# Kernel tuning notes

Measured on AMD Instinct MI355X. Metric: run time of the kernel, lower is better.

The kernel has to match this reference:

```python
import jax, jax.numpy as jnp
import numpy as np

PI = jnp.float32(3.14159265359)  # same truncated constant as the torch source
LOG_2PI = jnp.log(2.0 * PI)
STAB = 0.001  # covariance stabilizer added before inversion in the original


def _decoder(z, W1, b1, W2, b2, W3, b3, W4, b4):
    # f: Linear(z_dim,64)-ELU-Linear(64,128)-ELU-Linear(128,256)-ELU-Linear(256,784)-Sigmoid
    h = jax.nn.elu(z @ W1.T + b1)
    h = jax.nn.elu(h @ W2.T + b2)
    h = jax.nn.elu(h @ W3.T + b3)
    return jax.nn.sigmoid(h @ W4.T + b4)


def setup_inputs() -> dict:
    key = jax.random.key(0)
    ks = jax.random.split(key, 6)
    N, K, D, Z = 512, 256, 784, 2

    def lin(k, fan_in, fan_out):
        k1, k2 = jax.random.split(k)
        lim = 1.0 / np.sqrt(fan_in)
        W = jax.random.uniform(k1, (fan_out, fan_in), minval=-lim, maxval=lim, dtype=jnp.float32)
        b = jax.random.uniform(k2, (fan_out,), minval=-lim, maxval=lim, dtype=jnp.float32)
        return W, b

    W1, b1 = lin(ks[0], Z, 64)
    W2, b2 = lin(ks[1], 64, 128)
    W3, b3 = lin(ks[2], 128, 256)
    W4, b4 = lin(ks[3], 256, D)
    X = jax.random.uniform(ks[4], (N, D), dtype=jnp.float32)   # image pixels in [0,1)
    z = jax.random.normal(ks[5], (K, Z), dtype=jnp.float32)    # latent MC samples
    log_std = jnp.zeros((1,), dtype=jnp.float32)               # self.log_std_ = tensor([0.0])
    return dict(X=X, z=z, log_std=log_std, W1=W1, b1=b1, W2=W2, b2=b2,
                W3=W3, b3=b3, W4=W4, b4=b4)


def reference(X, z, log_std, W1, b1, W2, b2, W3, b3, W4, b4):
    # expected_log_likelihood(X, z) == objective(X, z, variational=False)
    N, D = X.shape
    K, Z = z.shape
    s = jnp.exp(log_std[0])  # isotropic likelihood variance (covariance = s * I_D)

    # --- log_likelihood: MVN log-prob with covariance s*I_D (closed form of det/inverse) ---
    params = _decoder(z, W1, b1, W2, b2, W3, b3, W4, b4)           # (K, D)
    diffs = X[:, None, :] - params[None, :, :]                      # (N, K, D) dominant traffic
    quad = jnp.sum(diffs * diffs, axis=-1) / (s + STAB)             # inv((s+eps)*I) = I/(s+eps)
    log_norm = -0.5 * D * LOG_2PI - 0.5 * (D * log_std[0])          # log det(s*I_D) = D*log s
    ll = log_norm - 0.5 * quad                                      # (N, K)

    # --- log_prior: MVN log-prob with identity covariance (stabilized inverse: I/1.001) ---
    log_prior = -0.5 * Z * LOG_2PI - 0.5 * jnp.sum(z * z, axis=-1) / (1.0 + STAB)  # (K,)

    # --- importance weights computed under no_grad in the original ---
    sg = jax.lax.stop_gradient
    ll_c = sg(ll)
    lp_c = sg(log_prior)
    m = jnp.max(ll_c)
    ll_s = ll_c - m                                                 # (N, K)
    log_joint_s = ll_s + lp_c[None, :]                              # (N, K)
    evidence_s = jnp.exp(ll_s).sum(axis=-1) / K                     # (N,)
    log_evidence_s = jnp.log(evidence_s)
    log_posteriors = (log_joint_s - log_evidence_s[:, None]).T      # (K, N)
    iw = jnp.exp(log_posteriors - lp_c[:, None])                    # (K, N), constants

    ell = (iw.T * ll).sum(axis=-1) / K                              # (N,)
    return ell.sum() / N
```

## Files before the change

kernel.cpp:

```cpp
#include <hip/hip_runtime.h>
#include <math.h>

#define LOG_2PI 1.8378770664093453f

__device__ __forceinline__ float elu_f(float x) {
    return x > 0.0f ? x : expm1f(x);
}
__device__ __forceinline__ float sigmoid_f(float x) {
    return 1.0f / (1.0f + expf(-x));
}

__global__ __launch_bounds__(256) void decoder_kernel(
    const float* __restrict__ z,
    const float* __restrict__ W1, const float* __restrict__ b1,
    const float* __restrict__ W2, const float* __restrict__ b2,
    const float* __restrict__ W3, const float* __restrict__ b3,
    const float* __restrict__ W4, const float* __restrict__ b4,
    float* __restrict__ PT)
{
    __shared__ __align__(16) float h1[4][64];
    __shared__ __align__(16) float h2[4][128];
    __shared__ __align__(16) float h3[4][256];

    const int t  = threadIdx.x;
    const int kt = blockIdx.x >> 2;
    const int jq = blockIdx.x & 3;
    const int k0 = kt * 4;

    {
        int kl = t >> 6, o = t & 63;
        float z0 = z[(k0 + kl) * 2 + 0];
        float z1 = z[(k0 + kl) * 2 + 1];
        float v = fmaf(z0, W1[o * 2 + 0], fmaf(z1, W1[o * 2 + 1], b1[o]));
        h1[kl][o] = elu_f(v);
    }
    __syncthreads();

    for (int idx = t; idx < 512; idx += 256) {
        int kl = idx >> 7, o = idx & 127;
        const float4* wr = reinterpret_cast<const float4*>(W2 + o * 64);
        const float4* hr = reinterpret_cast<const float4*>(h1[kl]);
        float acc = b2[o];
        #pragma unroll
        for (int i = 0; i < 16; ++i) {
            float4 w = wr[i]; float4 a = hr[i];
            acc = fmaf(w.x, a.x, acc); acc = fmaf(w.y, a.y, acc);
            acc = fmaf(w.z, a.z, acc); acc = fmaf(w.w, a.w, acc);
        }
        h2[kl][o] = elu_f(acc);
    }
    __syncthreads();

    for (int idx = t; idx < 1024; idx += 256) {
        int kl = idx >> 8, o = idx & 255;
        const float4* wr = reinterpret_cast<const float4*>(W3 + o * 128);
        const float4* hr = reinterpret_cast<const float4*>(h2[kl]);
        float acc = b3[o];
        #pragma unroll
        for (int i = 0; i < 32; ++i) {
            float4 w = wr[i]; float4 a = hr[i];
            acc = fmaf(w.x, a.x, acc); acc = fmaf(w.y, a.y, acc);
            acc = fmaf(w.z, a.z, acc); acc = fmaf(w.w, a.w, acc);
        }
        h3[kl][o] = elu_f(acc);
    }
    __syncthreads();

    if (t < 196) {
        const int j = jq * 196 + t;
        const float4* wr = reinterpret_cast<const float4*>(W4 + j * 256);
        const float4* h0 = reinterpret_cast<const float4*>(h3[0]);
        const float4* hA = reinterpret_cast<const float4*>(h3[1]);
        const float4* hB = reinterpret_cast<const float4*>(h3[2]);
        const float4* hC = reinterpret_cast<const float4*>(h3[3]);
        float bb = b4[j];
        float a0 = bb, a1 = bb, a2 = bb, a3 = bb;
        #pragma unroll 8
        for (int i = 0; i < 64; ++i) {
            float4 w = wr[i];
            float4 x0 = h0[i], x1 = hA[i], x2 = hB[i], x3 = hC[i];
            a0 = fmaf(w.x, x0.x, a0); a0 = fmaf(w.y, x0.y, a0);
            a0 = fmaf(w.z, x0.z, a0); a0 = fmaf(w.w, x0.w, a0);
            a1 = fmaf(w.x, x1.x, a1); a1 = fmaf(w.y, x1.y, a1);
            a1 = fmaf(w.z, x1.z, a1); a1 = fmaf(w.w, x1.w, a1);
            a2 = fmaf(w.x, x2.x, a2); a2 = fmaf(w.y, x2.y, a2);
            a2 = fmaf(w.z, x2.z, a2); a2 = fmaf(w.w, x2.w, a2);
            a3 = fmaf(w.x, x3.x, a3); a3 = fmaf(w.y, x3.y, a3);
            a3 = fmaf(w.z, x3.z, a3); a3 = fmaf(w.w, x3.w, a3);
        }
        float4 r = make_float4(sigmoid_f(a0), sigmoid_f(a1),
                               sigmoid_f(a2), sigmoid_f(a3));
        *reinterpret_cast<float4*>(PT + j * 256 + k0) = r;
    }
}

__global__ __launch_bounds__(256) void quad_part_kernel(
    const float* __restrict__ X, const float* __restrict__ log_std,
    const float* __restrict__ PT, float* __restrict__ part)
{
    __shared__ __align__(16) float Xs[4][784];
    __shared__ float red[4][16][17];

    const int t  = threadIdx.x;
    const int nb = blockIdx.x & 127;
    const int bq = blockIdx.x >> 7;
    const int n0 = nb * 4;

    {
        const float4* X4  = reinterpret_cast<const float4*>(X + n0 * 784);
        float4*       Xs4 = reinterpret_cast<float4*>(&Xs[0][0]);
        for (int i = t; i < 784; i += 256) Xs4[i] = X4[i];
    }
    __syncthreads();

    const int w    = t >> 6, l = t & 63;
    const int kv   = l & 15;
    const int dsub = l >> 4;
    const int db   = w * 196 + dsub * 49;

    const float4* P4 = reinterpret_cast<const float4*>(PT) + bq * 16 + kv;

    float a00=0.f,a01=0.f,a02=0.f,a03=0.f;
    float a10=0.f,a11=0.f,a12=0.f,a13=0.f;
    float a20=0.f,a21=0.f,a22=0.f,a23=0.f;
    float a30=0.f,a31=0.f,a32=0.f,a33=0.f;

    #pragma unroll 7
    for (int i = 0; i < 49; ++i) {
        const int d = db + i;
        float4 p = P4[d * 64];
        float x0 = Xs[0][d], x1 = Xs[1][d], x2 = Xs[2][d], x3 = Xs[3][d];
        float e;
        e = x0-p.x; a00=fmaf(e,e,a00);  e = x0-p.y; a01=fmaf(e,e,a01);
        e = x0-p.z; a02=fmaf(e,e,a02);  e = x0-p.w; a03=fmaf(e,e,a03);
        e = x1-p.x; a10=fmaf(e,e,a10);  e = x1-p.y; a11=fmaf(e,e,a11);
        e = x1-p.z; a12=fmaf(e,e,a12);  e = x1-p.w; a13=fmaf(e,e,a13);
        e = x2-p.x; a20=fmaf(e,e,a20);  e = x2-p.y; a21=fmaf(e,e,a21);
        e = x2-p.z; a22=fmaf(e,e,a22);  e = x2-p.w; a23=fmaf(e,e,a23);
        e = x3-p.x; a30=fmaf(e,e,a30);  e = x3-p.y; a31=fmaf(e,e,a31);
        e = x3-p.z; a32=fmaf(e,e,a32);  e = x3-p.w; a33=fmaf(e,e,a33);
    }

    #define RED2(v) v += __shfl_xor(v, 16); v += __shfl_xor(v, 32);
    RED2(a00) RED2(a01) RED2(a02) RED2(a03)
    RED2(a10) RED2(a11) RED2(a12) RED2(a13)
    RED2(a20) RED2(a21) RED2(a22) RED2(a23)
    RED2(a30) RED2(a31) RED2(a32) RED2(a33)
    #undef RED2

    if (l < 16) {
        float* rr = red[w][l];
        rr[0]=a00;  rr[1]=a01;  rr[2]=a02;  rr[3]=a03;
        rr[4]=a10;  rr[5]=a11;  rr[6]=a12;  rr[7]=a13;
        rr[8]=a20;  rr[9]=a21;  rr[10]=a22; rr[11]=a23;
        rr[12]=a30; rr[13]=a31; rr[14]=a32; rr[15]=a33;
    }
    __syncthreads();

    if (l < 16) {
        const int r4 = w * 4;
        float q0 = red[0][l][r4+0] + red[1][l][r4+0] + red[2][l][r4+0] + red[3][l][r4+0];
        float q1 = red[0][l][r4+1] + red[1][l][r4+1] + red[2][l][r4+1] + red[3][l][r4+1];
        float q2 = red[0][l][r4+2] + red[1][l][r4+2] + red[2][l][r4+2] + red[3][l][r4+2];
        float q3 = red[0][l][r4+3] + red[1][l][r4+3] + red[2][l][r4+3] + red[3][l][r4+3];

        float ls  = log_std[0];
        float s   = expf(ls);
        float inv = 1.0f / (s + 0.001f);
        float log_norm = -0.5f * 784.0f * LOG_2PI - 0.5f * 784.0f * ls;

        float ll0 = log_norm - 0.5f * q0 * inv;
        float ll1 = log_norm - 0.5f * q1 * inv;
        float ll2 = log_norm - 0.5f * q2 * inv;
        float ll3 = log_norm - 0.5f * q3 * inv;

        float m = fmaxf(fmaxf(ll0, ll1), fmaxf(ll2, ll3));
        #pragma unroll
        for (int off = 1; off < 16; off <<= 1)
            m = fmaxf(m, __shfl_xor(m, off));

        float e0 = expf(ll0 - m), e1 = expf(ll1 - m);
        float e2 = expf(ll2 - m), e3 = expf(ll3 - m);
        float s0 = (e0 + e1) + (e2 + e3);
        float s1 = fmaf(e0, ll0, fmaf(e1, ll1, fmaf(e2, ll2, e3 * ll3)));
        #pragma unroll
        for (int off = 1; off < 16; off <<= 1) {
            s0 += __shfl_xor(s0, off);
            s1 += __shfl_xor(s1, off);
        }

        if (l == 0) {
            float* pp = part + ((n0 + w) * 4 + bq) * 3;
            pp[0] = m; pp[1] = s0; pp[2] = s1;
        }
    }
}

__global__ __launch_bounds__(256) void finalize_kernel(
    const float* __restrict__ part, float* __restrict__ out)
{
    __shared__ float red[4];
    const int t = threadIdx.x;
    float v = 0.0f;
    #pragma unroll
    for (int h = 0; h < 2; ++h) {
        const float* pp = part + (t + h * 256) * 12;
        float M = fmaxf(fmaxf(pp[0], pp[3]), fmaxf(pp[6], pp[9]));
        float S0 = 0.0f, S1 = 0.0f;
        #pragma unroll
        for (int q = 0; q < 4; ++q) {
            float f = expf(pp[q * 3] - M);
            S0 = fmaf(pp[q * 3 + 1], f, S0);
            S1 = fmaf(pp[q * 3 + 2], f, S1);
        }
        v += S1 / S0;
    }
    for (int off = 32; off > 0; off >>= 1)
        v += __shfl_down(v, off);
    if ((t & 63) == 0) red[t >> 6] = v;
    __syncthreads();
    if (t == 0)
        out[0] = (red[0] + red[1] + red[2] + red[3]) * (1.0f / 512.0f);
}

extern "C" void kernel_launch(void* const* d_in, const int* in_sizes, int n_in,
                              void* d_out, int out_size, void* d_ws, size_t ws_size,
                              hipStream_t stream) {
    const float* X       = (const float*)d_in[0];
    const float* z       = (const float*)d_in[1];
    const float* log_std = (const float*)d_in[2];
    const float* W1      = (const float*)d_in[3];
    const float* b1      = (const float*)d_in[4];
    const float* W2      = (const float*)d_in[5];
    const float* b2      = (const float*)d_in[6];
    const float* W3      = (const float*)d_in[7];
    const float* b3      = (const float*)d_in[8];
    const float* W4      = (const float*)d_in[9];
    const float* b4      = (const float*)d_in[10];
    float* out = (float*)d_out;

    float* wsf  = (float*)d_ws;
    float* PT   = wsf;
    float* part = wsf + 200704;

    decoder_kernel<<<256, 256, 0, stream>>>(z, W1, b1, W2, b2, W3, b3, W4, b4, PT);
    quad_part_kernel<<<512, 256, 0, stream>>>(X, log_std, PT, part);
    finalize_kernel<<<1, 256, 0, stream>>>(part, out);
}
```

Measured before the change: 116.2 us.

## Fuse finalize into quad kernel via last-block counter; halve decoder batch per block

Removes the separate finalize launch: each quad_part block bumps a global atomic counter, and the last block to arrive performs the final cross-row reduction. The counter is reset inside the decoder kernel. The decoder also processes 2 latent samples per block instead of 4, doubling its grid to 512 blocks for more parallelism at the cost of rereading W4 twice as often. This trades one kernel launch for fences and atomics, plus extra weight traffic in the decoder.

```diff
diff --git a/kernel.cpp b/kernel.cpp
--- a/kernel.cpp
+++ b/kernel.cpp
@@ -16,18 +16,20 @@
     const float* __restrict__ W2, const float* __restrict__ b2,
     const float* __restrict__ W3, const float* __restrict__ b3,
     const float* __restrict__ W4, const float* __restrict__ b4,
-    float* __restrict__ PT)
+    float* __restrict__ PT, unsigned int* __restrict__ counter)
 {
-    __shared__ __align__(16) float h1[4][64];
-    __shared__ __align__(16) float h2[4][128];
-    __shared__ __align__(16) float h3[4][256];
+    __shared__ __align__(16) float h1[2][64];
+    __shared__ __align__(16) float h2[2][128];
+    __shared__ __align__(16) float h3[2][256];
 
     const int t  = threadIdx.x;
     const int kt = blockIdx.x >> 2;
     const int jq = blockIdx.x & 3;
-    const int k0 = kt * 4;
-
-    {
+    const int k0 = kt * 2;
+
+    if (blockIdx.x == 0 && t == 0) counter[0] = 0u;
+
+    if (t < 128) {
         int kl = t >> 6, o = t & 63;
         float z0 = z[(k0 + kl) * 2 + 0];
         float z1 = z[(k0 + kl) * 2 + 1];
@@ -36,8 +38,8 @@
     }
     __syncthreads();
 
-    for (int idx = t; idx < 512; idx += 256) {
-        int kl = idx >> 7, o = idx & 127;
+    {
+        int kl = t >> 7, o = t & 127;
         const float4* wr = reinterpret_cast<const float4*>(W2 + o * 64);
         const float4* hr = reinterpret_cast<const float4*>(h1[kl]);
         float acc = b2[o];
@@ -51,7 +53,7 @@
     }
     __syncthreads();
 
-    for (int idx = t; idx < 1024; idx += 256) {
+    for (int idx = t; idx < 512; idx += 256) {
         int kl = idx >> 8, o = idx & 255;
         const float4* wr = reinterpret_cast<const float4*>(W3 + o * 128);
         const float4* hr = reinterpret_cast<const float4*>(h2[kl]);
@@ -71,35 +73,31 @@
         const float4* wr = reinterpret_cast<const float4*>(W4 + j * 256);
         const float4* h0 = reinterpret_cast<const float4*>(h3[0]);
         const float4* hA = reinterpret_cast<const float4*>(h3[1]);
-        const float4* hB = reinterpret_cast<const float4*>(h3[2]);
-        const float4* hC = reinterpret_cast<const float4*>(h3[3]);
         float bb = b4[j];
-        float a0 = bb, a1 = bb, a2 = bb, a3 = bb;
+        float a0 = bb, a1 = bb;
         #pragma unroll 8
         for (int i = 0; i < 64; ++i) {
             float4 w = wr[i];
-            float4 x0 = h0[i], x1 = hA[i], x2 = hB[i], x3 = hC[i];
+            float4 x0 = h0[i], x1 = hA[i];
             a0 = fmaf(w.x, x0.x, a0); a0 = fmaf(w.y, x0.y, a0);
             a0 = fmaf(w.z, x0.z, a0); a0 = fmaf(w.w, x0.w, a0);
             a1 = fmaf(w.x, x1.x, a1); a1 = fmaf(w.y, x1.y, a1);
             a1 = fmaf(w.z, x1.z, a1); a1 = fmaf(w.w, x1.w, a1);
-            a2 = fmaf(w.x, x2.x, a2); a2 = fmaf(w.y, x2.y, a2);
-            a2 = fmaf(w.z, x2.z, a2); a2 = fmaf(w.w, x2.w, a2);
-            a3 = fmaf(w.x, x3.x, a3); a3 = fmaf(w.y, x3.y, a3);
-            a3 = fmaf(w.z, x3.z, a3); a3 = fmaf(w.w, x3.w, a3);
-        }
-        float4 r = make_float4(sigmoid_f(a0), sigmoid_f(a1),
-                               sigmoid_f(a2), sigmoid_f(a3));
-        *reinterpret_cast<float4*>(PT + j * 256 + k0) = r;
+        }
+        float2 r = make_float2(sigmoid_f(a0), sigmoid_f(a1));
+        *reinterpret_cast<float2*>(PT + j * 256 + k0) = r;
     }
 }
 
 __global__ __launch_bounds__(256) void quad_part_kernel(
     const float* __restrict__ X, const float* __restrict__ log_std,
-    const float* __restrict__ PT, float* __restrict__ part)
+    const float* __restrict__ PT, float* __restrict__ part,
+    unsigned int* __restrict__ counter, float* __restrict__ out)
 {
     __shared__ __align__(16) float Xs[4][784];
     __shared__ float red[4][16][17];
+    __shared__ int is_last;
+    __shared__ float red2[4];
 
     const int t  = threadIdx.x;
     const int nb = blockIdx.x & 127;
@@ -191,36 +189,52 @@
 
         if (l == 0) {
             float* pp = part + ((n0 + w) * 4 + bq) * 3;
-            pp[0] = m; pp[1] = s0; pp[2] = s1;
-        }
-    }
-}
-
-__global__ __launch_bounds__(256) void finalize_kernel(
-    const float* __restrict__ part, float* __restrict__ out)
-{
-    __shared__ float red[4];
-    const int t = threadIdx.x;
+            __hip_atomic_store(&pp[0], m,  __ATOMIC_RELAXED, __HIP_MEMORY_SCOPE_AGENT);
+            __hip_atomic_store(&pp[1], s0, __ATOMIC_RELAXED, __HIP_MEMORY_SCOPE_AGENT);
+            __hip_atomic_store(&pp[2], s1, __ATOMIC_RELAXED, __HIP_MEMORY_SCOPE_AGENT);
+        }
+    }
+    __syncthreads();
+
+    if (t == 0) {
+        __threadfence();
+        unsigned int old = atomicAdd(counter, 1u);
+        is_last = (old == 511u);
+    }
+    __syncthreads();
+    if (!is_last) return;
+
+    __threadfence();
     float v = 0.0f;
     #pragma unroll
     for (int h = 0; h < 2; ++h) {
         const float* pp = part + (t + h * 256) * 12;
-        float M = fmaxf(fmaxf(pp[0], pp[3]), fmaxf(pp[6], pp[9]));
-        float S0 = 0.0f, S1 = 0.0f;
-        #pragma unroll
-        for (int q = 0; q < 4; ++q) {
-            float f = expf(pp[q * 3] - M);
-            S0 = fmaf(pp[q * 3 + 1], f, S0);
-            S1 = fmaf(pp[q * 3 + 2], f, S1);
-        }
+        float m0 = __hip_atomic_load(&pp[0],  __ATOMIC_RELAXED, __HIP_MEMORY_SCOPE_AGENT);
+        float s00 = __hip_atomic_load(&pp[1], __ATOMIC_RELAXED, __HIP_MEMORY_SCOPE_AGENT);
+        float s10 = __hip_atomic_load(&pp[2], __ATOMIC_RELAXED, __HIP_MEMORY_SCOPE_AGENT);
+        float m1 = __hip_atomic_load(&pp[3],  __ATOMIC_RELAXED, __HIP_MEMORY_SCOPE_AGENT);
+        float s01 = __hip_atomic_load(&pp[4], __ATOMIC_RELAXED, __HIP_MEMORY_SCOPE_AGENT);
+        float s11 = __hip_atomic_load(&pp[5], __ATOMIC_RELAXED, __HIP_MEMORY_SCOPE_AGENT);
+        float m2 = __hip_atomic_load(&pp[6],  __ATOMIC_RELAXED, __HIP_MEMORY_SCOPE_AGENT);
+        float s02 = __hip_atomic_load(&pp[7], __ATOMIC_RELAXED, __HIP_MEMORY_SCOPE_AGENT);
+        float s12 = __hip_atomic_load(&pp[8], __ATOMIC_RELAXED, __HIP_MEMORY_SCOPE_AGENT);
+        float m3 = __hip_atomic_load(&pp[9],  __ATOMIC_RELAXED, __HIP_MEMORY_SCOPE_AGENT);
+        float s03 = __hip_atomic_load(&pp[10],__ATOMIC_RELAXED, __HIP_MEMORY_SCOPE_AGENT);
+        float s13 = __hip_atomic_load(&pp[11],__ATOMIC_RELAXED, __HIP_MEMORY_SCOPE_AGENT);
+
+        float M = fmaxf(fmaxf(m0, m1), fmaxf(m2, m3));
+        float f0 = expf(m0 - M), f1 = expf(m1 - M);
+        float f2 = expf(m2 - M), f3 = expf(m3 - M);
+        float S0 = fmaf(s00, f0, fmaf(s01, f1, fmaf(s02, f2, s03 * f3)));
+        float S1 = fmaf(s10, f0, fmaf(s11, f1, fmaf(s12, f2, s13 * f3)));
         v += S1 / S0;
     }
     for (int off = 32; off > 0; off >>= 1)
         v += __shfl_down(v, off);
-    if ((t & 63) == 0) red[t >> 6] = v;
+    if ((t & 63) == 0) red2[t >> 6] = v;
     __syncthreads();
     if (t == 0)
-        out[0] = (red[0] + red[1] + red[2] + red[3]) * (1.0f / 512.0f);
+        out[0] = (red2[0] + red2[1] + red2[2] + red2[3]) * (1.0f / 512.0f);
 }
 
 extern "C" void kernel_launch(void* const* d_in, const int* in_sizes, int n_in,
@@ -239,11 +253,12 @@
     const float* b4      = (const float*)d_in[10];
     float* out = (float*)d_out;
 
-    float* wsf  = (float*)d_ws;
-    float* PT   = wsf;
-    float* part = wsf + 200704;
-
-    decoder_kernel<<<256, 256, 0, stream>>>(z, W1, b1, W2, b2, W3, b3, W4, b4, PT);
-    quad_part_kernel<<<512, 256, 0, stream>>>(X, log_std, PT, part);
-    finalize_kernel<<<1, 256, 0, stream>>>(part, out);
-}
+    float*        wsf     = (float*)d_ws;
+    float*        PT      = wsf;
+    float*        part    = wsf + 200704;
+    unsigned int* counter = (unsigned int*)(wsf + 206848);
+
+    decoder_kernel<<<512, 256, 0, stream>>>(z, W1, b1, W2, b2, W3, b3, W4, b4,
+                                            PT, counter);
+    quad_part_kernel<<<512, 256, 0, stream>>>(X, log_std, PT, part, counter, out);
+}
```

Result: slower. 127.8 us (+10.0%).
